# Kernel tuning notes

Measured on AMD Instinct MI355X. Metric: run time of the kernel, lower is better.

## Reference

```python
import jax, jax.numpy as jnp
import numpy as np
from jax import lax

# physiological constants from the source module
DT = 1.0
TAU_L = 10.0
G_B = 0.6
G_L = 1.0 / TAU_L
LAMBDA_MAX = 0.35
STEPS = int(50 / DT)

IN_SIZE, HID, OUT, BATCH = 1024, 2048, 512, 4096


def setup_inputs() -> dict:
    key = jax.random.key(0)
    k1, k2, k3, k4, k5, k6 = jax.random.split(key, 6)
    psp = jax.random.uniform(k1, (IN_SIZE, BATCH), dtype=jnp.float32)  # |mm(spikes,kernel)| is >=0
    label = jax.random.uniform(k2, (BATCH, OUT), dtype=jnp.float32)    # teaching current I
    # Linear params init: uniform(-0.1, 0.1) as in the torch module
    W_h = jax.random.uniform(k3, (HID, IN_SIZE), minval=-0.1, maxval=0.1, dtype=jnp.float32)
    b_h = jax.random.uniform(k4, (HID,), minval=-0.1, maxval=0.1, dtype=jnp.float32)
    W_o = jax.random.uniform(k5, (OUT, HID), minval=-0.1, maxval=0.1, dtype=jnp.float32)
    b_o = jax.random.uniform(k6, (OUT,), minval=-0.1, maxval=0.1, dtype=jnp.float32)
    return {"psp": psp, "label": label, "W_h": W_h, "b_h": b_h, "W_o": W_o, "b_o": b_o}


def reference(psp, label, W_h, b_h, W_o, b_o):
    a = DT / TAU_L
    gr = G_B / G_L  # = 6.0
    x = psp.T  # [B, in] -- Hidden_layer transposes basal_input
    # psp is constant over the time loop, so the hidden basal GEMM hoists out
    basal_V_h = x @ W_h.T + b_h  # [B, HID]
    soma_h0 = jnp.zeros_like(basal_V_h)
    soma_o0 = jnp.zeros((x.shape[0], W_o.shape[0]), dtype=x.dtype)

    def step(carry, _):
        soma_h, soma_o = carry
        # hidden two-compartment leaky integration
        soma_h = soma_h + a * (-soma_h + gr * (basal_V_h - soma_h))
        rate_h = LAMBDA_MAX * jax.nn.sigmoid(soma_h)  # [B, HID]
        basal_V_o = rate_h @ W_o.T + b_o              # [B, OUT]
        # output layer, training (test=False) branch: nudged by teaching current I=label
        soma_o = soma_o + a * (-soma_o + gr * (basal_V_o - soma_o) + label - soma_o)
        return (soma_h, soma_o), None

    (soma_h, soma_o), _ = lax.scan(step, (soma_h0, soma_o0), None, length=STEPS)
    return LAMBDA_MAX * jax.nn.sigmoid(soma_o)  # out_layer.spike_rate, [B, OUT]
```

## Files before the change

### kernel.cpp

```cpp
#include <hip/hip_runtime.h>
#include <hip/hip_bf16.h>


typedef __bf16 bf16_t;
typedef __bf16 bf16x8 __attribute__((ext_vector_type(8)));
typedef __bf16 bf16x4v __attribute__((ext_vector_type(4)));
typedef float f32x4 __attribute__((ext_vector_type(4)));
typedef float f32x16 __attribute__((ext_vector_type(16)));

#define GLD_TO_LDS16(gp, lp)                                            \
  __builtin_amdgcn_global_load_lds(                                     \
      (__attribute__((address_space(1))) void*)(void*)(gp),             \
      (__attribute__((address_space(3))) void*)(lp), 16, 0, 0)

__global__ __launch_bounds__(256) void prep(
    const float* __restrict__ psp, bf16_t* __restrict__ pspT,
    const float4* __restrict__ w1, bf16x4v* __restrict__ o1, int n1,
    const float4* __restrict__ w2, bf16x4v* __restrict__ o2, int n2) {
  __shared__ float tile[64][65];
  const int tid = threadIdx.x;
  const int b = blockIdx.x;
  const int c0 = (b & 63) * 64;
  const int r0 = (b >> 6) * 64;
  const int tx = tid & 63;
  const int ty = tid >> 6;
#pragma unroll
  for (int i = 0; i < 16; ++i) {
    const int r = ty + i * 4;
    tile[r][tx] = psp[(size_t)(r0 + r) * 4096 + c0 + tx];
  }
  const int base = b * 768 + tid;
#pragma unroll
  for (int i = 0; i < 3; ++i) {
    const int idx = base + i * 256;
    const float4 v = (idx < n1) ? w1[idx] : w2[idx - n1];
    bf16x4v o;
    o.x = (bf16_t)v.x; o.y = (bf16_t)v.y; o.z = (bf16_t)v.z; o.w = (bf16_t)v.w;
    if (idx < n1) o1[idx] = o;
    else if (idx - n1 < n2) o2[idx - n1] = o;
  }
  __syncthreads();
#pragma unroll
  for (int i = 0; i < 16; ++i) {
    const int r = ty + i * 4;
    pspT[(size_t)(c0 + r) * 1024 + r0 + tx] = (bf16_t)tile[tx][r];
  }
}

__global__ __launch_bounds__(256, 2) void gemm1_nt(
    const bf16_t* __restrict__ A, const bf16_t* __restrict__ Bt,
    const float* __restrict__ bias, bf16_t* __restrict__ C,
    int M, int N, int K) {
  __shared__ __align__(16) bf16_t sA[2][128 * 64];
  __shared__ __align__(16) bf16_t sB[2][128 * 64];

  const int tid = threadIdx.x;
  const int wave = tid >> 6;
  const int lane = tid & 63;
  const int bm = blockIdx.x * 128;
  const int bn = blockIdx.y * 128;
  const int wm = (wave & 1) * 64;
  const int wn = (wave >> 1) * 64;

  f32x16 acc[2][2] = {};

  const int srow8 = lane >> 3;
  const int gseg = (lane & 7) ^ srow8;
  const bf16_t* Ag = A + (size_t)(bm + wave * 32 + srow8) * K + gseg * 8;
  const bf16_t* Bg = Bt + (size_t)(bn + wave * 32 + srow8) * K + gseg * 8;
  const int dst = wave * 2048;

  const int col = lane & 31;
  const int g = lane >> 5;
  const int NT = K / 128;

  for (int t = 0; t < NT; ++t) {
    const int k0 = t * 128;
#pragma unroll
    for (int p = 0; p < 2; ++p) {
#pragma unroll
      for (int c = 0; c < 4; ++c) {
        GLD_TO_LDS16(Ag + k0 + p * 64 + (size_t)(c * 8) * K,
                     sA[p] + dst + c * 512);
        GLD_TO_LDS16(Bg + k0 + p * 64 + (size_t)(c * 8) * K,
                     sB[p] + dst + c * 512);
      }
    }
    __syncthreads();

#pragma unroll
    for (int p = 0; p < 2; ++p) {
#pragma unroll
      for (int ks = 0; ks < 4; ++ks) {
        const int q = ks * 2 + g;
        bf16x8 av[2], bv[2];
#pragma unroll
        for (int i = 0; i < 2; ++i) {
          const int rr = wm + i * 32 + col;
          av[i] = *(const bf16x8*)(sA[p] + rr * 64 + ((q ^ (rr & 7)) * 8));
        }
#pragma unroll
        for (int j = 0; j < 2; ++j) {
          const int rr = wn + j * 32 + col;
          bv[j] = *(const bf16x8*)(sB[p] + rr * 64 + ((q ^ (rr & 7)) * 8));
        }
#pragma unroll
        for (int i = 0; i < 2; ++i)
#pragma unroll
          for (int j = 0; j < 2; ++j)
            acc[i][j] = __builtin_amdgcn_mfma_f32_32x32x16_bf16(
                av[i], bv[j], acc[i][j], 0, 0, 0);
      }
    }
    __syncthreads();
  }

  const int rbase = 4 * g;
#pragma unroll
  for (int j = 0; j < 2; ++j) {
    const int gn = bn + wn + j * 32 + col;
    const float bj = bias[gn];
#pragma unroll
    for (int i = 0; i < 2; ++i) {
#pragma unroll
      for (int r = 0; r < 16; ++r) {
        const int gm = bm + wm + i * 32 + (r & 3) + 8 * (r >> 2) + rbase;
        const float z = 0.8571428571428571f * (acc[i][j][r] + bj);
        C[(size_t)gm * N + gn] = (bf16_t)(0.35f / (1.0f + __expf(-z)));
      }
    }
  }
}

__global__ __launch_bounds__(256, 2) void gemm2_nt(
    const bf16_t* __restrict__ A, const bf16_t* __restrict__ Bt,
    const float* __restrict__ bias, const float* __restrict__ lbl,
    float* __restrict__ out, int M, int N, int K) {
  __shared__ __align__(16) bf16_t sA[4][64 * 64];
  __shared__ __align__(16) bf16_t sB[4][64 * 64];

  const int tid = threadIdx.x;
  const int wave = tid >> 6;
  const int lane = tid & 63;
  const int bm = blockIdx.x * 64;
  const int bn = blockIdx.y * 64;
  const int wm = (wave & 1) * 32;
  const int wn = (wave >> 1) * 32;

  f32x4 acc[2][2] = {};

  const int srow8 = lane >> 3;
  const int gseg = (lane & 7) ^ srow8;
  const bf16_t* Ag = A + (size_t)(bm + wave * 16 + srow8) * K + gseg * 8;
  const bf16_t* Bg = Bt + (size_t)(bn + wave * 16 + srow8) * K + gseg * 8;
  const int dst = wave * 1024;

  const int fr = lane & 15;
  const int qh = lane >> 4;
  const int NT = K / 256;

  for (int t = 0; t < NT; ++t) {
    const int k0 = t * 256;
#pragma unroll
    for (int p = 0; p < 4; ++p) {
#pragma unroll
      for (int c = 0; c < 2; ++c) {
        GLD_TO_LDS16(Ag + k0 + p * 64 + (size_t)(c * 8) * K,
                     sA[p] + dst + c * 512);
        GLD_TO_LDS16(Bg + k0 + p * 64 + (size_t)(c * 8) * K,
                     sB[p] + dst + c * 512);
      }
    }
    __syncthreads();

#pragma unroll
    for (int ks = 0; ks < 8; ++ks) {
      const int pnl = ks >> 1;
      const int q2 = (ks * 4 + qh) & 7;
      bf16x8 av[2], bv[2];
#pragma unroll
      for (int i = 0; i < 2; ++i) {
        const int ra = wm + i * 16 + fr;
        av[i] = *(const bf16x8*)(sA[pnl] + ra * 64 + ((q2 ^ (ra & 7)) * 8));
      }
#pragma unroll
      for (int j = 0; j < 2; ++j) {
        const int rb = wn + j * 16 + fr;
        bv[j] = *(const bf16x8*)(sB[pnl] + rb * 64 + ((q2 ^ (rb & 7)) * 8));
      }
#pragma unroll
      for (int i = 0; i < 2; ++i)
#pragma unroll
        for (int j = 0; j < 2; ++j)
          acc[i][j] = __builtin_amdgcn_mfma_f32_16x16x32_bf16(
              av[i], bv[j], acc[i][j], 0, 0, 0);
    }
    __syncthreads();
  }

  const int cm0 = qh * 4;
#pragma unroll
  for (int j = 0; j < 2; ++j) {
    const int gn = bn + wn + j * 16 + fr;
    const float bj = bias[gn];
#pragma unroll
    for (int i = 0; i < 2; ++i) {
#pragma unroll
      for (int r = 0; r < 4; ++r) {
        const int gm = bm + wm + i * 16 + cm0 + r;
        const float z =
            0.75f * (acc[i][j][r] + bj) + 0.125f * lbl[(size_t)gm * N + gn];
        out[(size_t)gm * N + gn] = 0.35f / (1.0f + __expf(-z));
      }
    }
  }
}

extern "C" void kernel_launch(void* const* d_in, const int* in_sizes, int n_in,
                              void* d_out, int out_size, void* d_ws, size_t ws_size,
                              hipStream_t stream) {
  constexpr int IN = 1024, HID = 2048, OUT = 512, B = 4096;
  const float* psp = (const float*)d_in[0];
  const float* lbl = (const float*)d_in[1];
  const float* W_h = (const float*)d_in[2];
  const float* b_h = (const float*)d_in[3];
  const float* W_o = (const float*)d_in[4];
  const float* b_o = (const float*)d_in[5];
  float* out = (float*)d_out;

  bf16_t* Whb = (bf16_t*)d_ws;
  bf16_t* Wob = Whb + (size_t)HID * IN;
  bf16_t* pspT = Wob + (size_t)OUT * HID;
  bf16_t* Rm = pspT + (size_t)B * IN;

  prep<<<1024, 256, 0, stream>>>(
      psp, pspT, (const float4*)W_h, (bf16x4v*)Whb, HID * IN / 4,
      (const float4*)W_o, (bf16x4v*)Wob, OUT * HID / 4);
  gemm1_nt<<<dim3(B / 128, HID / 128), 256, 0, stream>>>(
      pspT, Whb, b_h, Rm, B, HID, IN);
  gemm2_nt<<<dim3(B / 64, OUT / 64), 256, 0, stream>>>(
      Rm, Wob, b_o, lbl, out, B, OUT, HID);
}
```

Measured before the change: 127.0 us.

## Quantize first GEMM operands to FP8 and use scaled MFMA 32x32x64

Converts psp (transposed) and W_h to FP8 in the prep kernel and rewrites gemm1 to load byte tiles and issue the MI355 mfma_scale f8f6f4 32x32x64 instruction with unit scales. This halves the operand bytes moved and doubles the MFMA throughput of the larger GEMM. It also adds s_setprio around the MFMA block. FP8 loses precision on inputs and weights, which risks accuracy, and K is now hardcoded to 1024.

```diff
diff --git a/kernel.cpp b/kernel.cpp
--- a/kernel.cpp
+++ b/kernel.cpp
@@ -7,16 +7,23 @@
 typedef __bf16 bf16x4v __attribute__((ext_vector_type(4)));
 typedef float f32x4 __attribute__((ext_vector_type(4)));
 typedef float f32x16 __attribute__((ext_vector_type(16)));
+typedef int i32x4 __attribute__((ext_vector_type(4)));
+typedef int i32x8 __attribute__((ext_vector_type(8)));
 
 #define GLD_TO_LDS16(gp, lp)                                            \
   __builtin_amdgcn_global_load_lds(                                     \
       (__attribute__((address_space(1))) void*)(void*)(gp),             \
       (__attribute__((address_space(3))) void*)(lp), 16, 0, 0)
 
+__device__ inline int pk4_fp8(float x, float y, float z, float w) {
+  int lo = __builtin_amdgcn_cvt_pk_fp8_f32(x, y, 0, false);
+  return __builtin_amdgcn_cvt_pk_fp8_f32(z, w, lo, true);
+}
+
 __global__ __launch_bounds__(256) void prep(
-    const float* __restrict__ psp, bf16_t* __restrict__ pspT,
-    const float4* __restrict__ w1, bf16x4v* __restrict__ o1, int n1,
-    const float4* __restrict__ w2, bf16x4v* __restrict__ o2, int n2) {
+    const float* __restrict__ psp, unsigned char* __restrict__ pspT8,
+    const float4* __restrict__ wh, int* __restrict__ wh8,
+    const float4* __restrict__ wo, bf16x4v* __restrict__ wob) {
   __shared__ float tile[64][65];
   const int tid = threadIdx.x;
   const int b = blockIdx.x;
@@ -29,30 +36,40 @@
     const int r = ty + i * 4;
     tile[r][tx] = psp[(size_t)(r0 + r) * 4096 + c0 + tx];
   }
-  const int base = b * 768 + tid;
-#pragma unroll
-  for (int i = 0; i < 3; ++i) {
-    const int idx = base + i * 256;
-    const float4 v = (idx < n1) ? w1[idx] : w2[idx - n1];
+  {
+    const int i1 = b * 512 + tid;
+#pragma unroll
+    for (int u = 0; u < 2; ++u) {
+      const int idx = i1 + u * 256;
+      const float4 v = wh[idx];
+      wh8[idx] = pk4_fp8(v.x, v.y, v.z, v.w);
+    }
+  }
+  {
+    const int i2 = b * 256 + tid;
+    const float4 v = wo[i2];
     bf16x4v o;
     o.x = (bf16_t)v.x; o.y = (bf16_t)v.y; o.z = (bf16_t)v.z; o.w = (bf16_t)v.w;
-    if (idx < n1) o1[idx] = o;
-    else if (idx - n1 < n2) o2[idx - n1] = o;
+    wob[i2] = o;
   }
   __syncthreads();
-#pragma unroll
-  for (int i = 0; i < 16; ++i) {
-    const int r = ty + i * 4;
-    pspT[(size_t)(c0 + r) * 1024 + r0 + tx] = (bf16_t)tile[tx][r];
+  const int brow0 = tid >> 4;
+  const int c4 = (tid & 15) * 4;
+#pragma unroll
+  for (int i = 0; i < 4; ++i) {
+    const int brow = brow0 + i * 16;
+    const int packed = pk4_fp8(tile[c4][brow], tile[c4 + 1][brow],
+                               tile[c4 + 2][brow], tile[c4 + 3][brow]);
+    *(int*)(pspT8 + (size_t)(c0 + brow) * 1024 + r0 + c4) = packed;
   }
 }
 
 __global__ __launch_bounds__(256, 2) void gemm1_nt(
-    const bf16_t* __restrict__ A, const bf16_t* __restrict__ Bt,
+    const unsigned char* __restrict__ A8, const unsigned char* __restrict__ B8,
     const float* __restrict__ bias, bf16_t* __restrict__ C,
     int M, int N, int K) {
-  __shared__ __align__(16) bf16_t sA[2][128 * 64];
-  __shared__ __align__(16) bf16_t sB[2][128 * 64];
+  __shared__ __align__(16) unsigned char sA[2][128 * 128];
+  __shared__ __align__(16) unsigned char sB[2][128 * 128];
 
   const int tid = threadIdx.x;
   const int wave = tid >> 6;
@@ -66,51 +83,59 @@
 
   const int srow8 = lane >> 3;
   const int gseg = (lane & 7) ^ srow8;
-  const bf16_t* Ag = A + (size_t)(bm + wave * 32 + srow8) * K + gseg * 8;
-  const bf16_t* Bg = Bt + (size_t)(bn + wave * 32 + srow8) * K + gseg * 8;
-  const int dst = wave * 2048;
+  const unsigned char* Ag =
+      A8 + (size_t)(bm + wave * 32 + srow8) * 1024 + gseg * 16;
+  const unsigned char* Bg =
+      B8 + (size_t)(bn + wave * 32 + srow8) * 1024 + gseg * 16;
+  const int dst = wave * 4096;
 
   const int col = lane & 31;
   const int g = lane >> 5;
-  const int NT = K / 128;
-
-  for (int t = 0; t < NT; ++t) {
-    const int k0 = t * 128;
-#pragma unroll
-    for (int p = 0; p < 2; ++p) {
+
+  for (int t = 0; t < 4; ++t) {
+    const int kb = t * 256;
+#pragma unroll
+    for (int h = 0; h < 2; ++h) {
 #pragma unroll
       for (int c = 0; c < 4; ++c) {
-        GLD_TO_LDS16(Ag + k0 + p * 64 + (size_t)(c * 8) * K,
-                     sA[p] + dst + c * 512);
-        GLD_TO_LDS16(Bg + k0 + p * 64 + (size_t)(c * 8) * K,
-                     sB[p] + dst + c * 512);
-      }
-    }
-    __syncthreads();
-
-#pragma unroll
-    for (int p = 0; p < 2; ++p) {
-#pragma unroll
-      for (int ks = 0; ks < 4; ++ks) {
-        const int q = ks * 2 + g;
-        bf16x8 av[2], bv[2];
-#pragma unroll
-        for (int i = 0; i < 2; ++i) {
-          const int rr = wm + i * 32 + col;
-          av[i] = *(const bf16x8*)(sA[p] + rr * 64 + ((q ^ (rr & 7)) * 8));
-        }
-#pragma unroll
-        for (int j = 0; j < 2; ++j) {
-          const int rr = wn + j * 32 + col;
-          bv[j] = *(const bf16x8*)(sB[p] + rr * 64 + ((q ^ (rr & 7)) * 8));
-        }
-#pragma unroll
-        for (int i = 0; i < 2; ++i)
-#pragma unroll
-          for (int j = 0; j < 2; ++j)
-            acc[i][j] = __builtin_amdgcn_mfma_f32_32x32x16_bf16(
-                av[i], bv[j], acc[i][j], 0, 0, 0);
-      }
+        GLD_TO_LDS16(Ag + kb + h * 128 + (size_t)(c * 8) * 1024,
+                     sA[h] + dst + c * 1024);
+        GLD_TO_LDS16(Bg + kb + h * 128 + (size_t)(c * 8) * 1024,
+                     sB[h] + dst + c * 1024);
+      }
+    }
+    __syncthreads();
+
+#pragma unroll
+    for (int p = 0; p < 4; ++p) {
+      const int h = p >> 1;
+      const int s0 = (p & 1) * 4 + 2 * g;
+      i32x8 av[2], bv[2];
+#pragma unroll
+      for (int i = 0; i < 2; ++i) {
+        const int rr = wm + i * 32 + col;
+        const unsigned char* base = sA[h] + rr * 128;
+        const i32x4 lo = *(const i32x4*)(base + ((s0 ^ (rr & 7)) * 16));
+        const i32x4 hi = *(const i32x4*)(base + (((s0 + 1) ^ (rr & 7)) * 16));
+        av[i] = __builtin_shufflevector(lo, hi, 0, 1, 2, 3, 4, 5, 6, 7);
+      }
+#pragma unroll
+      for (int j = 0; j < 2; ++j) {
+        const int rr = wn + j * 32 + col;
+        const unsigned char* base = sB[h] + rr * 128;
+        const i32x4 lo = *(const i32x4*)(base + ((s0 ^ (rr & 7)) * 16));
+        const i32x4 hi = *(const i32x4*)(base + (((s0 + 1) ^ (rr & 7)) * 16));
+        bv[j] = __builtin_shufflevector(lo, hi, 0, 1, 2, 3, 4, 5, 6, 7);
+      }
+      __builtin_amdgcn_s_setprio(1);
+#pragma unroll
+      for (int i = 0; i < 2; ++i)
+#pragma unroll
+        for (int j = 0; j < 2; ++j)
+          acc[i][j] = __builtin_amdgcn_mfma_scale_f32_32x32x64_f8f6f4(
+              av[i], bv[j], acc[i][j], 0, 0,
+              0, 0x7F7F7F7F, 0, 0x7F7F7F7F);
+      __builtin_amdgcn_s_setprio(0);
     }
     __syncthreads();
   }
@@ -228,16 +253,16 @@
   const float* b_o = (const float*)d_in[5];
   float* out = (float*)d_out;
 
-  bf16_t* Whb = (bf16_t*)d_ws;
-  bf16_t* Wob = Whb + (size_t)HID * IN;
-  bf16_t* pspT = Wob + (size_t)OUT * HID;
-  bf16_t* Rm = pspT + (size_t)B * IN;
+  unsigned char* Whb8 = (unsigned char*)d_ws;
+  bf16_t* Wob = (bf16_t*)(Whb8 + (size_t)HID * IN);
+  unsigned char* pspT8 = (unsigned char*)(Wob + (size_t)OUT * HID);
+  bf16_t* Rm = (bf16_t*)(pspT8 + (size_t)B * IN);
 
   prep<<<1024, 256, 0, stream>>>(
-      psp, pspT, (const float4*)W_h, (bf16x4v*)Whb, HID * IN / 4,
-      (const float4*)W_o, (bf16x4v*)Wob, OUT * HID / 4);
+      psp, pspT8, (const float4*)W_h, (int*)Whb8, (const float4*)W_o,
+      (bf16x4v*)Wob);
   gemm1_nt<<<dim3(B / 128, HID / 128), 256, 0, stream>>>(
-      pspT, Whb, b_h, Rm, B, HID, IN);
+      pspT8, Whb8, b_h, Rm, B, HID, IN);
   gemm2_nt<<<dim3(B / 64, OUT / 64), 256, 0, stream>>>(
       Rm, Wob, b_o, lbl, out, B, OUT, HID);
 }
```

After: 117.3 us. -7.6%, faster.
